# Kernel tuning notes

Measured on AMD Instinct MI355X. Metric: run time of the kernel, lower is better.

Reference implementation:

```python
import jax, jax.numpy as jnp
import numpy as np

B, L, D, O, E, K = 2, 2048, 2048, 2048, 8, 2


def setup_inputs() -> dict:
    key = jax.random.key(0)
    k1, k2, k3, k4 = jax.random.split(key, 4)
    scale = float(np.sqrt(1.0 / D))
    x = jax.random.normal(k1, (B, L, D), dtype=jnp.float32)
    # weight init: uniform(-sqrt(1/D), sqrt(1/D)), shape (E, O, D) as in torch
    weight = jax.random.uniform(k2, (E, O, D), dtype=jnp.float32, minval=-scale, maxval=scale)
    # torch inits bias to zeros; use small random values so the bias path is exercised
    bias = jax.random.normal(k3, (E, O), dtype=jnp.float32) * 0.02
    indices = jax.random.randint(k4, (B, L, K), 0, E, dtype=jnp.int32)
    return {"x": x, "weight": weight, "bias": bias, "indices": indices}


def reference(x, weight, bias, indices):
    # Faithful math: out[b,l,j,:] = weight[indices[b,l,j]] @ x[b,l,:] + bias[indices[b,l,j]]
    # Efficient expression: compute all-expert projections once (dense GEMM),
    # then gather the routed expert per (token, slot). This avoids materializing
    # the per-token [B,L,K,O,D] gathered weight tensor the torch code creates.
    y_all = jnp.einsum('bld,eod->bleo', x, weight)          # (B, L, E, O)
    y = jnp.take_along_axis(y_all, indices[..., None], axis=2)  # (B, L, K, O)
    return y + bias[indices]                                 # bias gather (B, L, K, O)
```

## Files before the change

### kernel.cpp

```cpp
#include <hip/hip_runtime.h>
#include <hip/hip_bf16.h>

#define Ddim 2048
#define Odim 2048
#define Edim 8
#define NTOK 4096
#define NSLOT 8192
#define CAP NSLOT
#define BM 128
#define BN 128
#define BK 64
#define NTK 32
#define MAXMT 16
#define NTN 16

typedef __attribute__((ext_vector_type(8))) short bf16x8;
typedef __attribute__((ext_vector_type(4))) float f32x4;
typedef __attribute__((ext_vector_type(8))) unsigned short ushort8;

__device__ __forceinline__ unsigned short f2bf(float f) {
  unsigned u = __builtin_bit_cast(unsigned, f);
  u += 0x7FFFu + ((u >> 16) & 1u);
  return (unsigned short)(u >> 16);
}

__global__ void prep_kernel(const float* __restrict__ x, const float* __restrict__ w,
                            const int* __restrict__ idx,
                            unsigned short* __restrict__ xb, unsigned short* __restrict__ wb,
                            int* __restrict__ perm, int* __restrict__ count) {
  const int b = blockIdx.x, tid = threadIdx.x;
  if (b == 0) {
    __shared__ int cnt[Edim];
    if (tid < Edim) cnt[tid] = 0;
    __syncthreads();
    for (int s = tid; s < NSLOT; s += 256) {
      int e = idx[s];
      int pos = atomicAdd(&cnt[e], 1);
      perm[e * CAP + pos] = s;
    }
    __syncthreads();
    for (int e = 0; e < Edim; ++e) {
      int c = cnt[e];
      int pad = (c + BM - 1) & ~(BM - 1);
      for (int p = c + tid; p < pad; p += 256) perm[e * CAP + p] = 0;
    }
    if (tid < Edim) count[tid] = cnt[tid];
    return;
  }
  long u = (long)(b - 1) * 256 + tid;
  const long n8x = (long)NTOK * Ddim / 8;
  const float* src; unsigned short* dst; long uu;
  if (u < n8x) { src = x; dst = xb; uu = u; }
  else { src = w; dst = wb; uu = u - n8x; }
  const float4* p = (const float4*)src;
  float4 a = p[2 * uu], c4 = p[2 * uu + 1];
  ushort8 o;
  o[0] = f2bf(a.x);  o[1] = f2bf(a.y);  o[2] = f2bf(a.z);  o[3] = f2bf(a.w);
  o[4] = f2bf(c4.x); o[5] = f2bf(c4.y); o[6] = f2bf(c4.z); o[7] = f2bf(c4.w);
  *(ushort8*)(dst + uu * 8) = o;
}

__device__ __forceinline__ void gload16(const unsigned short* g, unsigned short* l) {
  __builtin_amdgcn_global_load_lds(
      (const __attribute__((address_space(1))) void*)g,
      (__attribute__((address_space(3))) void*)l, 16, 0, 0);
}

__global__ __launch_bounds__(256, 2) void moe_gemm(
    const unsigned short* __restrict__ xb, const unsigned short* __restrict__ wb,
    const float* __restrict__ bias, const int* __restrict__ perm,
    const int* __restrict__ count, float* __restrict__ out) {
  const int nt = blockIdx.x, e = blockIdx.y, mt = blockIdx.z;
  const int ne = count[e];
  if (mt * BM >= ne) return;

  __shared__ unsigned short lA[2][BM * BK];
  __shared__ unsigned short lB[2][BN * BK];

  const int tid = threadIdx.x;
  const int wid = tid >> 6, lane = tid & 63;
  const int wr = wid >> 1, wc = wid & 1;
  const int r15 = lane & 15, hi = lane >> 4, r7 = lane & 7;

  const int sSlot = (((tid & 7) ^ ((tid >> 3) & 7)) << 3);
  const unsigned short* aP[4]; const unsigned short* bP[4];
  #pragma unroll
  for (int j = 0; j < 4; ++j) {
    int rl = j * 32 + (tid >> 3);
    int s = perm[e * CAP + mt * BM + rl];
    aP[j] = xb + (long)(s >> 1) * Ddim + sSlot;
    bP[j] = wb + ((long)e * Odim + nt * BN + rl) * Ddim + sSlot;
  }
  unsigned short* dA0 = &lA[0][wid * 512]; unsigned short* dA1 = &lA[1][wid * 512];
  unsigned short* dB0 = &lB[0][wid * 512]; unsigned short* dB1 = &lB[1][wid * 512];

  #pragma unroll
  for (int j = 0; j < 4; ++j) gload16(aP[j], dA0 + j * 2048);
  #pragma unroll
  for (int j = 0; j < 4; ++j) gload16(bP[j], dB0 + j * 2048);
  #pragma unroll
  for (int j = 0; j < 4; ++j) gload16(bP[j] + BK, dB1 + j * 2048);

  f32x4 acc[4][4];
  #pragma unroll
  for (int m = 0; m < 4; ++m)
    #pragma unroll
    for (int n = 0; n < 4; ++n) acc[m][n] = (f32x4){0.f, 0.f, 0.f, 0.f};

  const int rowA0 = wr * 64 + r15;
  const int rowB0 = wc * 64 + r15;
  const int s0 = ((hi ^ r7) << 3);
  const int s1 = (((4 + hi) ^ r7) << 3);

  for (int t = 0; t < NTK; ++t) {
    const int c = t & 1;
    const int akt = (t + 1 < NTK) ? (t + 1) : (NTK - 1);
    const int bkt = (t + 2 < NTK) ? (t + 2) : (NTK - 1);
    const unsigned short* A  = c ? lA[1] : lA[0];
    const unsigned short* Bv = c ? lB[1] : lB[0];
    unsigned short* stA = c ? dA0 : dA1;
    unsigned short* stB = c ? dB1 : dB0;

    asm volatile("s_waitcnt vmcnt(4)" ::: "memory");
    __builtin_amdgcn_s_barrier();

    bf16x8 bf[4][2], a0, a1;
    #pragma unroll
    for (int n = 0; n < 4; ++n) {
      bf[n][0] = *(const bf16x8*)&Bv[(rowB0 + n * 16) * BK + s0];
      bf[n][1] = *(const bf16x8*)&Bv[(rowB0 + n * 16) * BK + s1];
    }
    a0 = *(const bf16x8*)&A[rowA0 * BK + s0];
    a1 = *(const bf16x8*)&A[rowA0 * BK + s1];
    gload16(aP[0] + akt * BK, stA);
    gload16(aP[1] + akt * BK, stA + 2048);
    __builtin_amdgcn_s_barrier();
    asm volatile("s_waitcnt lgkmcnt(0)" ::: "memory");
    __builtin_amdgcn_s_setprio(1);
    #pragma unroll
    for (int n = 0; n < 4; ++n) {
      acc[0][n] = __builtin_amdgcn_mfma_f32_16x16x32_bf16(a0, bf[n][0], acc[0][n], 0, 0, 0);
      acc[0][n] = __builtin_amdgcn_mfma_f32_16x16x32_bf16(a1, bf[n][1], acc[0][n], 0, 0, 0);
    }
    __builtin_amdgcn_s_setprio(0);

    a0 = *(const bf16x8*)&A[(rowA0 + 16) * BK + s0];
    a1 = *(const bf16x8*)&A[(rowA0 + 16) * BK + s1];
    gload16(aP[2] + akt * BK, stA + 4096);
    gload16(aP[3] + akt * BK, stA + 6144);
    __builtin_amdgcn_s_barrier();
    asm volatile("s_waitcnt lgkmcnt(0)" ::: "memory");
    __builtin_amdgcn_s_setprio(1);
    #pragma unroll
    for (int n = 0; n < 4; ++n) {
      acc[1][n] = __builtin_amdgcn_mfma_f32_16x16x32_bf16(a0, bf[n][0], acc[1][n], 0, 0, 0);
      acc[1][n] = __builtin_amdgcn_mfma_f32_16x16x32_bf16(a1, bf[n][1], acc[1][n], 0, 0, 0);
    }
    __builtin_amdgcn_s_setprio(0);

    a0 = *(const bf16x8*)&A[(rowA0 + 32) * BK + s0];
    a1 = *(const bf16x8*)&A[(rowA0 + 32) * BK + s1];
    gload16(bP[0] + bkt * BK, stB);
    gload16(bP[1] + bkt * BK, stB + 2048);
    __builtin_amdgcn_s_barrier();
    asm volatile("s_waitcnt lgkmcnt(0)" ::: "memory");
    __builtin_amdgcn_s_setprio(1);
    #pragma unroll
    for (int n = 0; n < 4; ++n) {
      acc[2][n] = __builtin_amdgcn_mfma_f32_16x16x32_bf16(a0, bf[n][0], acc[2][n], 0, 0, 0);
      acc[2][n] = __builtin_amdgcn_mfma_f32_16x16x32_bf16(a1, bf[n][1], acc[2][n], 0, 0, 0);
    }
    __builtin_amdgcn_s_setprio(0);

    a0 = *(const bf16x8*)&A[(rowA0 + 48) * BK + s0];
    a1 = *(const bf16x8*)&A[(rowA0 + 48) * BK + s1];
    gload16(bP[2] + bkt * BK, stB + 4096);
    gload16(bP[3] + bkt * BK, stB + 6144);
    __builtin_amdgcn_s_barrier();
    asm volatile("s_waitcnt lgkmcnt(0)" ::: "memory");
    __builtin_amdgcn_s_setprio(1);
    #pragma unroll
    for (int n = 0; n < 4; ++n) {
      acc[3][n] = __builtin_amdgcn_mfma_f32_16x16x32_bf16(a0, bf[n][0], acc[3][n], 0, 0, 0);
      acc[3][n] = __builtin_amdgcn_mfma_f32_16x16x32_bf16(a1, bf[n][1], acc[3][n], 0, 0, 0);
    }
    __builtin_amdgcn_s_setprio(0);
  }

  const int rowBase = mt * BM;
  #pragma unroll
  for (int m = 0; m < 4; ++m) {
    int sIdx[4]; bool ok[4];
    #pragma unroll
    for (int j = 0; j < 4; ++j) {
      int rloc = wr * 64 + m * 16 + hi * 4 + j;
      ok[j] = (rowBase + rloc) < ne;
      sIdx[j] = ok[j] ? perm[e * CAP + rowBase + rloc] : 0;
    }
    #pragma unroll
    for (int n = 0; n < 4; ++n) {
      int colG = nt * BN + wc * 64 + n * 16 + r15;
      float bv = bias[e * Odim + colG];
      #pragma unroll
      for (int j = 0; j < 4; ++j)
        if (ok[j]) out[(long)sIdx[j] * Odim + colG] = acc[m][n][j] + bv;
    }
  }
}

extern "C" void kernel_launch(void* const* d_in, const int* in_sizes, int n_in,
                              void* d_out, int out_size, void* d_ws,
                              size_t ws_size, hipStream_t stream) {
  const float* x = (const float*)d_in[0];
  const float* w = (const float*)d_in[1];
  const float* bias = (const float*)d_in[2];
  const int* idx = (const int*)d_in[3];
  float* out = (float*)d_out;

  char* ws = (char*)d_ws;
  unsigned short* xb = (unsigned short*)ws;
  unsigned short* wb = (unsigned short*)(ws + (size_t)16 * 1024 * 1024);
  int* perm = (int*)(ws + (size_t)80 * 1024 * 1024);
  int* count = (int*)(ws + (size_t)80 * 1024 * 1024 + 256 * 1024);

  const int n8tot = (NTOK * Ddim + Edim * Odim * Ddim) / 8;
  prep_kernel<<<n8tot / 256 + 1, 256, 0, stream>>>(x, w, idx, xb, wb, perm, count);
  moe_gemm<<<dim3(NTN, Edim, MAXMT), 256, 0, stream>>>(xb, wb, bias, perm, count, out);
}
```

Measured before the change: 159.0 us.

## Enlarge MoE GEMM tile to 256x256 with 8 waves and restaged pipeline

Doubles the block tile in both M and N (BM=BN=256), moves to 512 threads laid out as 2x4 waves each owning 128x64 outputs, and rewrites the K-loop into a two-tile unrolled schedule. A fragments are loaded in groups of four and B fragments in pairs, with async LDS staging interleaved between MFMA groups. The aim is more reuse of each staged operand and less global/L2 traffic per FLOP. In exchange, LDS use doubles to 128KB per block, which limits occupancy to one block per CU. The grid also shrinks, so padding waste and tail imbalance across per-expert tiles can grow.

```diff
diff --git a/kernel.cpp b/kernel.cpp
--- a/kernel.cpp
+++ b/kernel.cpp
@@ -7,12 +7,12 @@
 #define NTOK 4096
 #define NSLOT 8192
 #define CAP NSLOT
-#define BM 128
-#define BN 128
+#define BM 256
+#define BN 256
 #define BK 64
 #define NTK 32
-#define MAXMT 16
-#define NTN 16
+#define MAXMT 8
+#define NTN 8
 
 typedef __attribute__((ext_vector_type(8))) short bf16x8;
 typedef __attribute__((ext_vector_type(4))) float f32x4;
@@ -66,7 +66,7 @@
       (__attribute__((address_space(3))) void*)l, 16, 0, 0);
 }
 
-__global__ __launch_bounds__(256, 2) void moe_gemm(
+__global__ __launch_bounds__(512, 2) void moe_gemm(
     const unsigned short* __restrict__ xb, const unsigned short* __restrict__ wb,
     const float* __restrict__ bias, const int* __restrict__ perm,
     const int* __restrict__ count, float* __restrict__ out) {
@@ -79,123 +79,117 @@
 
   const int tid = threadIdx.x;
   const int wid = tid >> 6, lane = tid & 63;
-  const int wr = wid >> 1, wc = wid & 1;
+  const int wr = wid >> 2, wc = wid & 3;
   const int r15 = lane & 15, hi = lane >> 4, r7 = lane & 7;
 
-  const int sSlot = (((tid & 7) ^ ((tid >> 3) & 7)) << 3);
-  const unsigned short* aP[4]; const unsigned short* bP[4];
+  const int srow = tid >> 3;
+  const int sslot = ((tid & 7) ^ (srow & 7)) << 3;
+  const unsigned short* aSrc[2][2];
+  const unsigned short* bSrc[2][2];
   #pragma unroll
-  for (int j = 0; j < 4; ++j) {
-    int rl = j * 32 + (tid >> 3);
-    int s = perm[e * CAP + mt * BM + rl];
-    aP[j] = xb + (long)(s >> 1) * Ddim + sSlot;
-    bP[j] = wb + ((long)e * Odim + nt * BN + rl) * Ddim + sSlot;
+  for (int h = 0; h < 2; ++h)
+    #pragma unroll
+    for (int i = 0; i < 2; ++i) {
+      int r = h * 128 + i * 64 + srow;
+      int s = perm[e * CAP + mt * BM + r];
+      aSrc[h][i] = xb + (long)(s >> 1) * Ddim + sslot;
+      bSrc[h][i] = wb + ((long)e * Odim + nt * BN + r) * Ddim + sslot;
+    }
+  unsigned short* dA[2] = { &lA[0][0], &lA[1][0] };
+  unsigned short* dB[2] = { &lB[0][0], &lB[1][0] };
+  const int wofs = wid * 512;
+
+#define STAGE_A(buf_, h_, koff_) do { \
+    gload16(aSrc[h_][0] + (koff_), dA[buf_] + (h_) * 8192 + wofs); \
+    gload16(aSrc[h_][1] + (koff_), dA[buf_] + (h_) * 8192 + 4096 + wofs); } while (0)
+#define STAGE_B(buf_, h_, koff_) do { \
+    gload16(bSrc[h_][0] + (koff_), dB[buf_] + (h_) * 8192 + wofs); \
+    gload16(bSrc[h_][1] + (koff_), dB[buf_] + (h_) * 8192 + 4096 + wofs); } while (0)
+
+  f32x4 acc[8][4];
+  #pragma unroll
+  for (int m = 0; m < 8; ++m)
+    #pragma unroll
+    for (int n = 0; n < 4; ++n) acc[m][n] = (f32x4){0.f, 0.f, 0.f, 0.f};
+
+  bf16x8 af[4][2], bf[4][2];
+  const int aRowB = (wr * 128 + r15) * BK;
+  const int bRowB = (wc * 64 + r15) * BK;
+  const int s0 = ((hi ^ r7) << 3);
+  const int s1 = s0 ^ 32;
+
+#define rdA4(mb_) do { _Pragma("unroll") for (int m_ = 0; m_ < 4; ++m_) { \
+    af[m_][0] = *(const bf16x8*)&Ac[aRowB + ((mb_) + m_) * 1024 + s0]; \
+    af[m_][1] = *(const bf16x8*)&Ac[aRowB + ((mb_) + m_) * 1024 + s1]; } } while (0)
+#define rdB2(nb_) do { _Pragma("unroll") for (int n_ = 0; n_ < 2; ++n_) { \
+    bf[(nb_) + n_][0] = *(const bf16x8*)&Bc[bRowB + ((nb_) + n_) * 1024 + s0]; \
+    bf[(nb_) + n_][1] = *(const bf16x8*)&Bc[bRowB + ((nb_) + n_) * 1024 + s1]; } } while (0)
+
+#define DO_MFMA(mb_, nb_) do { \
+    __builtin_amdgcn_s_setprio(1); \
+    _Pragma("unroll") for (int m_ = 0; m_ < 4; ++m_) \
+      _Pragma("unroll") for (int n_ = 0; n_ < 2; ++n_) { \
+        acc[(mb_) + m_][(nb_) + n_] = __builtin_amdgcn_mfma_f32_16x16x32_bf16( \
+            af[m_][0], bf[(nb_) + n_][0], acc[(mb_) + m_][(nb_) + n_], 0, 0, 0); \
+        acc[(mb_) + m_][(nb_) + n_] = __builtin_amdgcn_mfma_f32_16x16x32_bf16( \
+            af[m_][1], bf[(nb_) + n_][1], acc[(mb_) + m_][(nb_) + n_], 0, 0, 0); } \
+    __builtin_amdgcn_s_setprio(0); } while (0)
+
+  asm volatile("s_waitcnt vmcnt(0)" ::: "memory");
+  STAGE_B(0, 0, 0);
+  STAGE_B(0, 1, 0);
+  STAGE_A(0, 0, 0);
+  STAGE_A(0, 1, 0);
+  STAGE_B(1, 0, BK);
+  STAGE_B(1, 1, BK);
+
+#define TILE(t_, cur_) do { \
+    const unsigned short* Ac = dA[cur_]; const unsigned short* Bc = dB[cur_]; \
+    const int ka = ((t_) + 1 < NTK ? (t_) + 1 : NTK - 1) * BK; \
+    const int kb = ((t_) + 2 < NTK ? (t_) + 2 : NTK - 1) * BK; \
+    asm volatile("s_waitcnt vmcnt(4)" ::: "memory"); \
+    __builtin_amdgcn_s_barrier(); \
+     \
+    rdA4(0); rdB2(0); \
+    STAGE_A(1 - (cur_), 0, ka); \
+    __builtin_amdgcn_s_barrier(); \
+    asm volatile("s_waitcnt lgkmcnt(0)" ::: "memory"); \
+    DO_MFMA(0, 0); \
+    __builtin_amdgcn_s_barrier(); \
+     \
+    rdB2(2); \
+    STAGE_A(1 - (cur_), 1, ka); \
+    __builtin_amdgcn_s_barrier(); \
+    asm volatile("s_waitcnt lgkmcnt(0)" ::: "memory"); \
+    DO_MFMA(0, 2); \
+    __builtin_amdgcn_s_barrier(); \
+     \
+    rdA4(4); \
+    STAGE_B(cur_, 0, kb); \
+    __builtin_amdgcn_s_barrier(); \
+    asm volatile("s_waitcnt lgkmcnt(0)" ::: "memory"); \
+    DO_MFMA(4, 0); \
+    __builtin_amdgcn_s_barrier(); \
+     \
+    STAGE_B(cur_, 1, kb); \
+    __builtin_amdgcn_s_barrier(); \
+    DO_MFMA(4, 2); \
+  } while (0)
+
+  for (int t = 0; t < NTK; t += 2) {
+    TILE(t, 0);
+    TILE(t + 1, 1);
   }
-  unsigned short* dA0 = &lA[0][wid * 512]; unsigned short* dA1 = &lA[1][wid * 512];
-  unsigned short* dB0 = &lB[0][wid * 512]; unsigned short* dB1 = &lB[1][wid * 512];
-
+
+  const int rowBase = mt * BM + wr * 128;
   #pragma unroll
-  for (int j = 0; j < 4; ++j) gload16(aP[j], dA0 + j * 2048);
-  #pragma unroll
-  for (int j = 0; j < 4; ++j) gload16(bP[j], dB0 + j * 2048);
-  #pragma unroll
-  for (int j = 0; j < 4; ++j) gload16(bP[j] + BK, dB1 + j * 2048);
-
-  f32x4 acc[4][4];
-  #pragma unroll
-  for (int m = 0; m < 4; ++m)
-    #pragma unroll
-    for (int n = 0; n < 4; ++n) acc[m][n] = (f32x4){0.f, 0.f, 0.f, 0.f};
-
-  const int rowA0 = wr * 64 + r15;
-  const int rowB0 = wc * 64 + r15;
-  const int s0 = ((hi ^ r7) << 3);
-  const int s1 = (((4 + hi) ^ r7) << 3);
-
-  for (int t = 0; t < NTK; ++t) {
-    const int c = t & 1;
-    const int akt = (t + 1 < NTK) ? (t + 1) : (NTK - 1);
-    const int bkt = (t + 2 < NTK) ? (t + 2) : (NTK - 1);
-    const unsigned short* A  = c ? lA[1] : lA[0];
-    const unsigned short* Bv = c ? lB[1] : lB[0];
-    unsigned short* stA = c ? dA0 : dA1;
-    unsigned short* stB = c ? dB1 : dB0;
-
-    asm volatile("s_waitcnt vmcnt(4)" ::: "memory");
-    __builtin_amdgcn_s_barrier();
-
-    bf16x8 bf[4][2], a0, a1;
-    #pragma unroll
-    for (int n = 0; n < 4; ++n) {
-      bf[n][0] = *(const bf16x8*)&Bv[(rowB0 + n * 16) * BK + s0];
-      bf[n][1] = *(const bf16x8*)&Bv[(rowB0 + n * 16) * BK + s1];
-    }
-    a0 = *(const bf16x8*)&A[rowA0 * BK + s0];
-    a1 = *(const bf16x8*)&A[rowA0 * BK + s1];
-    gload16(aP[0] + akt * BK, stA);
-    gload16(aP[1] + akt * BK, stA + 2048);
-    __builtin_amdgcn_s_barrier();
-    asm volatile("s_waitcnt lgkmcnt(0)" ::: "memory");
-    __builtin_amdgcn_s_setprio(1);
-    #pragma unroll
-    for (int n = 0; n < 4; ++n) {
-      acc[0][n] = __builtin_amdgcn_mfma_f32_16x16x32_bf16(a0, bf[n][0], acc[0][n], 0, 0, 0);
-      acc[0][n] = __builtin_amdgcn_mfma_f32_16x16x32_bf16(a1, bf[n][1], acc[0][n], 0, 0, 0);
-    }
-    __builtin_amdgcn_s_setprio(0);
-
-    a0 = *(const bf16x8*)&A[(rowA0 + 16) * BK + s0];
-    a1 = *(const bf16x8*)&A[(rowA0 + 16) * BK + s1];
-    gload16(aP[2] + akt * BK, stA + 4096);
-    gload16(aP[3] + akt * BK, stA + 6144);
-    __builtin_amdgcn_s_barrier();
-    asm volatile("s_waitcnt lgkmcnt(0)" ::: "memory");
-    __builtin_amdgcn_s_setprio(1);
-    #pragma unroll
-    for (int n = 0; n < 4; ++n) {
-      acc[1][n] = __builtin_amdgcn_mfma_f32_16x16x32_bf16(a0, bf[n][0], acc[1][n], 0, 0, 0);
-      acc[1][n] = __builtin_amdgcn_mfma_f32_16x16x32_bf16(a1, bf[n][1], acc[1][n], 0, 0, 0);
-    }
-    __builtin_amdgcn_s_setprio(0);
-
-    a0 = *(const bf16x8*)&A[(rowA0 + 32) * BK + s0];
-    a1 = *(const bf16x8*)&A[(rowA0 + 32) * BK + s1];
-    gload16(bP[0] + bkt * BK, stB);
-    gload16(bP[1] + bkt * BK, stB + 2048);
-    __builtin_amdgcn_s_barrier();
-    asm volatile("s_waitcnt lgkmcnt(0)" ::: "memory");
-    __builtin_amdgcn_s_setprio(1);
-    #pragma unroll
-    for (int n = 0; n < 4; ++n) {
-      acc[2][n] = __builtin_amdgcn_mfma_f32_16x16x32_bf16(a0, bf[n][0], acc[2][n], 0, 0, 0);
-      acc[2][n] = __builtin_amdgcn_mfma_f32_16x16x32_bf16(a1, bf[n][1], acc[2][n], 0, 0, 0);
-    }
-    __builtin_amdgcn_s_setprio(0);
-
-    a0 = *(const bf16x8*)&A[(rowA0 + 48) * BK + s0];
-    a1 = *(const bf16x8*)&A[(rowA0 + 48) * BK + s1];
-    gload16(bP[2] + bkt * BK, stB + 4096);
-    gload16(bP[3] + bkt * BK, stB + 6144);
-    __builtin_amdgcn_s_barrier();
-    asm volatile("s_waitcnt lgkmcnt(0)" ::: "memory");
-    __builtin_amdgcn_s_setprio(1);
-    #pragma unroll
-    for (int n = 0; n < 4; ++n) {
-      acc[3][n] = __builtin_amdgcn_mfma_f32_16x16x32_bf16(a0, bf[n][0], acc[3][n], 0, 0, 0);
-      acc[3][n] = __builtin_amdgcn_mfma_f32_16x16x32_bf16(a1, bf[n][1], acc[3][n], 0, 0, 0);
-    }
-    __builtin_amdgcn_s_setprio(0);
-  }
-
-  const int rowBase = mt * BM;
-  #pragma unroll
-  for (int m = 0; m < 4; ++m) {
+  for (int m = 0; m < 8; ++m) {
     int sIdx[4]; bool ok[4];
     #pragma unroll
     for (int j = 0; j < 4; ++j) {
-      int rloc = wr * 64 + m * 16 + hi * 4 + j;
-      ok[j] = (rowBase + rloc) < ne;
-      sIdx[j] = ok[j] ? perm[e * CAP + rowBase + rloc] : 0;
+      int ri = rowBase + m * 16 + hi * 4 + j;
+      ok[j] = ri < ne;
+      sIdx[j] = ok[j] ? perm[e * CAP + ri] : 0;
     }
     #pragma unroll
     for (int n = 0; n < 4; ++n) {
@@ -225,5 +219,5 @@
 
   const int n8tot = (NTOK * Ddim + Edim * Odim * Ddim) / 8;
   prep_kernel<<<n8tot / 256 + 1, 256, 0, stream>>>(x, w, idx, xb, wb, perm, count);
-  moe_gemm<<<dim3(NTN, Edim, MAXMT), 256, 0, stream>>>(xb, wb, bias, perm, count, out);
-}
+  moe_gemm<<<dim3(NTN, Edim, MAXMT), 512, 0, stream>>>(xb, wb, bias, perm, count, out);
+}
```

Measured after the change: 179.5 us. 12.8% more time.
